# Kernel tuning notes

Measured on AMD Instinct MI355X. Metric: run time of the kernel, lower is better.

Reference implementation:

```python
import jax, jax.numpy as jnp
import numpy as np

B, L, E, H, D = 4, 2048, 2048, 16, 128
HALF = D // 2
EPS = 1e-6


def setup_inputs() -> dict:
    key = jax.random.key(0)
    ks = jax.random.split(key, 8)
    s = 1.0 / np.sqrt(E)
    x = jax.random.normal(ks[0], (B, L, E), dtype=jnp.float32)
    # causal boolean mask, True = attend
    attention_mask = jnp.tril(jnp.ones((L, L), dtype=bool))[None, None, :, :]
    attention_mask = jnp.broadcast_to(attention_mask, (B, 1, L, L))
    pos = jnp.arange(L, dtype=jnp.float32)[:, None]
    inv_freq = 1.0 / (10000.0 ** (jnp.arange(HALF, dtype=jnp.float32) / HALF))
    ang = pos * inv_freq[None, :]  # [L, HALF]
    cos = jnp.broadcast_to(jnp.cos(ang)[None], (B, L, HALF)).astype(jnp.float32)
    sin = jnp.broadcast_to(jnp.sin(ang)[None], (B, L, HALF)).astype(jnp.float32)
    Wq = jax.random.normal(ks[1], (H * D, E), dtype=jnp.float32) * s
    Wk = jax.random.normal(ks[2], (H * D, E), dtype=jnp.float32) * s
    Wv = jax.random.normal(ks[3], (H * D, E), dtype=jnp.float32) * s
    Wo = jax.random.normal(ks[4], (E, H * D), dtype=jnp.float32) * s
    q_norm_w = jnp.ones((D,), dtype=jnp.float32)
    k_norm_w = jnp.ones((D,), dtype=jnp.float32)
    return {"x": x, "attention_mask": attention_mask, "cos": cos, "sin": sin,
            "Wq": Wq, "Wk": Wk, "Wv": Wv, "Wo": Wo,
            "q_norm_w": q_norm_w, "k_norm_w": k_norm_w}


def _rmsnorm(t, w):
    # t: [B,H,L,D]; matches torch: x / sqrt(mean(x^2) + eps) * w
    ms = jnp.mean(t * t, axis=-1, keepdims=True)
    return w * (t * jax.lax.rsqrt(ms + EPS))


def _rope(t, cos, sin):
    # t: [B,H,L,D]; cos/sin: [B,L,HALF] -> [B,1,L,HALF]
    c = cos[:, None, :, :]
    s = sin[:, None, :, :]
    t1, t2 = t[..., :HALF], t[..., HALF:]
    return jnp.concatenate([t1 * c - t2 * s, t1 * s + t2 * c], axis=-1)


def reference(x, attention_mask, cos, sin, Wq, Wk, Wv, Wo, q_norm_w, k_norm_w):
    b, l, _ = x.shape
    q = (x @ Wq.T).reshape(b, l, H, D).transpose(0, 2, 1, 3)  # [B,H,L,D]
    k = (x @ Wk.T).reshape(b, l, H, D).transpose(0, 2, 1, 3)
    v = (x @ Wv.T).reshape(b, l, H, D).transpose(0, 2, 1, 3)
    q = _rope(_rmsnorm(q, q_norm_w), cos, sin)
    k = _rope(_rmsnorm(k, k_norm_w), cos, sin)
    scale = 1.0 / jnp.sqrt(jnp.asarray(D, dtype=x.dtype))
    scores = jnp.einsum('bhld,bhmd->bhlm', q, k) * scale  # [B,H,L,L]
    scores = jnp.where(attention_mask, scores, -jnp.inf)
    attn = jax.nn.softmax(scores, axis=-1)
    out = jnp.einsum('bhlm,bhmd->bhld', attn, v)  # [B,H,L,D]
    out = out.transpose(0, 2, 1, 3).reshape(b, l, H * D)
    return out @ Wo.T
```

## Files before the change

### kernel.cpp

```cpp
#include <hip/hip_runtime.h>
#include <hip/hip_bf16.h>
#include <stdint.h>

#define B_SZ 4
#define L_SEQ 2048
#define EMB 2048
#define NH 16
#define HD 128
#define BLROWS (B_SZ * L_SEQ)
#define BK 32

typedef __bf16 bf16;
typedef __bf16 bf16x8 __attribute__((ext_vector_type(8)));
typedef __bf16 bf16x4 __attribute__((ext_vector_type(4)));
typedef float f32x4 __attribute__((ext_vector_type(4)));

#define MFMA16(A, Bv, C) __builtin_amdgcn_mfma_f32_16x16x32_bf16(A, Bv, C, 0, 0, 0)

__device__ __forceinline__ void gll16(bf16* l, const bf16* g) {
  __builtin_amdgcn_global_load_lds(
      (const __attribute__((address_space(1))) unsigned int*)g,
      (__attribute__((address_space(3))) unsigned int*)l, 16, 0, 0);
}

__global__ __launch_bounds__(256) void f2bAll_kernel(
    const float* __restrict__ x, const float* __restrict__ w0,
    const float* __restrict__ w1, const float* __restrict__ w2,
    const float* __restrict__ w3, bf16* __restrict__ ox, bf16* __restrict__ o0,
    bf16* __restrict__ o1, bf16* __restrict__ o2, bf16* __restrict__ o3,
    int nx4, int nw4) {
  const int y = blockIdx.y;
  const float* in = (y == 0) ? x : (y == 1) ? w0 : (y == 2) ? w1
                    : (y == 3) ? w2 : w3;
  bf16* out = (y == 0) ? ox : (y == 1) ? o0 : (y == 2) ? o1
              : (y == 3) ? o2 : o3;
  const int n4 = (y == 0) ? nx4 : nw4;
  int i = blockIdx.x * blockDim.x + threadIdx.x;
  int stride = gridDim.x * blockDim.x;
  for (; i < n4; i += stride) {
    float4 v = ((const float4*)in)[i];
    bf16x4 o = {(bf16)v.x, (bf16)v.y, (bf16)v.z, (bf16)v.w};
    ((bf16x4*)out)[i] = o;
  }
}

template <int EPI, int BNT>
__global__ __launch_bounds__(512, 2) void gemm256(const bf16* __restrict__ A,
                                                  const bf16* __restrict__ Bm,
                                                  bf16* __restrict__ Cq,
                                                  bf16* __restrict__ Ck,
                                                  bf16* __restrict__ Cvt,
                                                  float* __restrict__ Cf,
                                                  int K) {
  constexpr int NB = BNT / 64;
  __shared__ bf16 Abuf[3][256 * BK];
  __shared__ bf16 Bbuf[3][BNT * BK];
  const int tid = threadIdx.x, lane = tid & 63, w = tid >> 6;
  const int wr = w >> 2, wc = w & 3;
  const int l15 = lane & 15;

  const int bx = blockIdx.x;
  const int bm = ((bx & 7) * 4 + ((bx >> 3) & 3)) * 256;
  const int bn = (bx >> 5) * BNT;
  const int NT = K / BK;

  const int idA0 = tid, idA1 = 512 + tid;
  const int ar0 = idA0 >> 2, ar1 = idA1 >> 2;
  const size_t aS0 = (size_t)(bm + ar0) * K + (((idA0 & 3) ^ ((ar0 >> 1) & 3)) * 8);
  const size_t aS1 = (size_t)(bm + ar1) * K + (((idA1 & 3) ^ ((ar1 >> 1) & 3)) * 8);
  const size_t bS0 = (size_t)(bn + ar0) * K + (((idA0 & 3) ^ ((ar0 >> 1) & 3)) * 8);
  const size_t bS1 = (size_t)(bn + ar1) * K + (((idA1 & 3) ^ ((ar1 >> 1) & 3)) * 8);
  const int ldsD0 = idA0 * 8, ldsD1 = idA1 * 8;

  const int eSw = ((lane >> 4) * 8) ^ (((l15 >> 1) & 3) << 3);
  int aoff[8], boff[NB];
#pragma unroll
  for (int m = 0; m < 8; m++) aoff[m] = (wr * 128 + m * 16 + l15) * BK + eSw;
#pragma unroll
  for (int n = 0; n < NB; n++) boff[n] = (wc * (BNT / 4) + n * 16 + l15) * BK + eSw;

  f32x4 acc[8][NB] = {};

  gll16(&Abuf[0][ldsD0], A + aS0);
  gll16(&Bbuf[0][ldsD0], Bm + bS0);
  gll16(&Abuf[0][ldsD1], A + aS1);
  if constexpr (BNT == 256) gll16(&Bbuf[0][ldsD1], Bm + bS1);
  gll16(&Abuf[1][ldsD0], A + aS0 + BK);
  gll16(&Bbuf[1][ldsD0], Bm + bS0 + BK);
  gll16(&Abuf[1][ldsD1], A + aS1 + BK);
  if constexpr (BNT == 256) gll16(&Bbuf[1][ldsD1], Bm + bS1 + BK);
  if constexpr (BNT == 256)
    asm volatile("s_waitcnt vmcnt(4)" ::: "memory");
  else
    asm volatile("s_waitcnt vmcnt(3)" ::: "memory");
  __builtin_amdgcn_s_barrier();
  asm volatile("" ::: "memory");

  int cur = 0, nxt = 2;
  for (int kt = 0; kt < NT; ++kt) {
    const bf16* __restrict__ Ab = Abuf[cur];
    const bf16* __restrict__ Bb = Bbuf[cur];
    const bool pre = (kt + 2 < NT);
    const size_t k2 = (size_t)(kt + 2) * BK;

    bf16x8 af[8], bq[NB];
#pragma unroll
    for (int m = 0; m < 8; m++) af[m] = *(const bf16x8*)&Ab[aoff[m]];
    bq[0] = *(const bf16x8*)&Bb[boff[0]];
    if constexpr (NB > 2) bq[1] = *(const bf16x8*)&Bb[boff[1]];
    if (pre) {
      gll16(&Abuf[nxt][ldsD0], A + aS0 + k2);
      gll16(&Bbuf[nxt][ldsD0], Bm + bS0 + k2);
    }
    asm volatile("s_waitcnt lgkmcnt(0)" ::: "memory");
    __builtin_amdgcn_sched_barrier(0);
    __builtin_amdgcn_s_setprio(1);
#pragma unroll
    for (int m = 0; m < 8; m++) acc[m][0] = MFMA16(af[m], bq[0], acc[m][0]);
    if constexpr (NB > 2) {
#pragma unroll
      for (int m = 0; m < 8; m++) acc[m][1] = MFMA16(af[m], bq[1], acc[m][1]);
    }
    __builtin_amdgcn_s_setprio(0);

    constexpr int n2 = (NB > 2) ? 2 : 1;
    bf16x8 b2 = *(const bf16x8*)&Bb[boff[n2]];
    bf16x8 b3;
    if constexpr (NB > 2) b3 = *(const bf16x8*)&Bb[boff[3]];
    if (pre) {
      gll16(&Abuf[nxt][ldsD1], A + aS1 + k2);
      if constexpr (BNT == 256) gll16(&Bbuf[nxt][ldsD1], Bm + bS1 + k2);
    }
    asm volatile("s_waitcnt lgkmcnt(0)" ::: "memory");
    __builtin_amdgcn_sched_barrier(0);
    __builtin_amdgcn_s_setprio(1);
#pragma unroll
    for (int m = 0; m < 8; m++) acc[m][n2] = MFMA16(af[m], b2, acc[m][n2]);
    if constexpr (NB > 2) {
#pragma unroll
      for (int m = 0; m < 8; m++) acc[m][3] = MFMA16(af[m], b3, acc[m][3]);
    }
    __builtin_amdgcn_s_setprio(0);

    if (kt < NT - 1) {
      if (pre) {
        if constexpr (BNT == 256)
          asm volatile("s_waitcnt vmcnt(4)" ::: "memory");
        else
          asm volatile("s_waitcnt vmcnt(3)" ::: "memory");
      } else {
        asm volatile("s_waitcnt vmcnt(0)" ::: "memory");
      }
      __builtin_amdgcn_s_barrier();
      asm volatile("" ::: "memory");
    }
    cur = (cur == 2) ? 0 : cur + 1;
    nxt = (nxt == 2) ? 0 : nxt + 1;
  }

  const int grow0 = bm + wr * 128 + (lane >> 4) * 4;
  const int gcol0 = bn + wc * (BNT / 4) + l15;
#pragma unroll
  for (int i = 0; i < 8; i++)
#pragma unroll
    for (int j = 0; j < NB; j++) {
      int grow = grow0 + i * 16;
      int gcol = gcol0 + j * 16;
      if (EPI == 1) {
#pragma unroll
        for (int r = 0; r < 4; r++)
          Cf[(size_t)(grow + r) * 2048 + gcol] = acc[i][j][r];
      } else {
        int mat = gcol >> 11, mcol = gcol & 2047;
        if (mat == 2) {
          int b = grow >> 11;
          bf16x4 pk = {(bf16)acc[i][j][0], (bf16)acc[i][j][1],
                       (bf16)acc[i][j][2], (bf16)acc[i][j][3]};
          *(bf16x4*)&Cvt[((size_t)(b * 2048 + mcol)) * 2048 + (grow & 2047)] = pk;
        } else {
          bf16* Cp = (mat == 0) ? Cq : Ck;
#pragma unroll
          for (int r = 0; r < 4; r++)
            Cp[(size_t)(grow + r) * 2048 + mcol] = (bf16)acc[i][j][r];
        }
      }
    }
}

__global__ __launch_bounds__(256) void normrope2_kernel(bf16* __restrict__ Tq,
                                                        bf16* __restrict__ Tk,
                                                        const float* __restrict__ wq,
                                                        const float* __restrict__ wk,
                                                        const float* __restrict__ cs,
                                                        const float* __restrict__ sn) {
  bf16* T = blockIdx.y ? Tk : Tq;
  const float* w = blockIdx.y ? wk : wq;
  int row = blockIdx.x * 4 + (threadIdx.x >> 6);
  int lane = threadIdx.x & 63;
  int bl = row >> 4;
  int h = row & 15;
  bf16* p = T + (size_t)bl * EMB + h * HD;
  float v1 = (float)p[lane];
  float v2 = (float)p[lane + 64];
  float ss = v1 * v1 + v2 * v2;
#pragma unroll
  for (int m = 32; m; m >>= 1) ss += __shfl_xor(ss, m, 64);
  float r = rsqrtf(ss * (1.0f / 128.0f) + 1e-6f);
  float n1 = v1 * r * w[lane];
  float n2 = v2 * r * w[lane + 64];
  float c = cs[(size_t)bl * 64 + lane];
  float s = sn[(size_t)bl * 64 + lane];
  p[lane]      = (bf16)(n1 * c - n2 * s);
  p[lane + 64] = (bf16)(n1 * s + n2 * c);
}

__device__ __forceinline__ void stage_kv(bf16* Ksb, bf16* Vsb,
                                         const bf16* gK, const bf16* gV,
                                         int kt, int w, int lane) {
#pragma unroll
  for (int i = 0; i < 4; i++) {
    int ck = i * 256 + w * 64 + lane;
    int kr = ck >> 4, kc = ck & 15;
    gll16(&Ksb[ck * 8], gK + (size_t)(kt * 64 + kr) * EMB + ((kc ^ (kr & 7)) * 8));
    int dr = ck >> 3, vc = ck & 7;
    gll16(&Vsb[ck * 8], gV + (size_t)dr * L_SEQ + kt * 64 + ((vc ^ (dr & 7)) * 8));
  }
}

__global__ __launch_bounds__(256) void fattn_kernel(const bf16* __restrict__ Q,
                                                    const bf16* __restrict__ K,
                                                    const bf16* __restrict__ Vt,
                                                    bf16* __restrict__ AO) {
  __shared__ bf16 Ks[2][64 * 128];
  __shared__ bf16 Vs[2][64 * 128];
  __shared__ bf16 Ps[4 * 16 * 64];
  const int tid = threadIdx.x, lane = tid & 63, w = tid >> 6;

  int id = blockIdx.x + blockIdx.y * 32;
  int bh = id & 63;
  int qt = 31 - (id >> 6);
  const int b = bh >> 4, h = bh & 15;
  const size_t base = (size_t)b * L_SEQ * EMB + h * HD;
  const bf16* gK = K + base;
  const bf16* gV = Vt + (size_t)(b * NH + h) * HD * L_SEQ;
  const int qrow0 = qt * 64 + w * 16;

  const float a_ = 0.08838834764831845f * 1.4426950408889634f;
  const float b_ = 12.0f * 1.4426950408889634f;

  bf16x8 qf[4];
  {
    const bf16* qp = Q + base + (size_t)(qrow0 + (lane & 15)) * EMB + ((lane >> 4) * 8);
#pragma unroll
    for (int c = 0; c < 4; c++) qf[c] = *(const bf16x8*)(qp + c * 32);
  }
  const bf16 one1 = (bf16)1.0f;
  const bf16x8 ones = {one1, one1, one1, one1, one1, one1, one1, one1};

  f32x4 O[8] = {};
  f32x4 lsum = {0.f, 0.f, 0.f, 0.f};
  const int qg0 = qrow0 + (lane >> 4) * 4;
  bf16* myP = Ps + w * 1024;

  stage_kv(Ks[0], Vs[0], gK, gV, 0, w, lane);
  asm volatile("s_waitcnt vmcnt(0)" ::: "memory");
  __builtin_amdgcn_s_barrier();
  asm volatile("" ::: "memory");

  for (int kt = 0; kt <= qt; kt++) {
    const int cur = kt & 1;
    if (kt < qt) stage_kv(Ks[cur ^ 1], Vs[cur ^ 1], gK, gV, kt + 1, w, lane);

    f32x4 S[4] = {};
    __builtin_amdgcn_s_setprio(1);
#pragma unroll
    for (int s = 0; s < 4; s++) {
      int row = s * 16 + (lane & 15);
#pragma unroll
      for (int c = 0; c < 4; c++) {
        int swc = (c * 4 + (lane >> 4)) ^ (row & 7);
        bf16x8 kf = *(const bf16x8*)&Ks[cur][row * 128 + swc * 8];
        S[s] = MFMA16(qf[c], kf, S[s]);
      }
    }
    __builtin_amdgcn_s_setprio(0);

    const bool diag = (kt == qt);
    const int prow = (lane >> 4) * 4;
#pragma unroll
    for (int s = 0; s < 4; s++) {
      int kg = kt * 64 + s * 16 + (lane & 15);
#pragma unroll
      for (int r = 0; r < 4; r++) {
        float e = exp2f(S[s][r] * a_ - b_);
        if (diag && kg > qg0 + r) e = 0.f;
        int row = prow + r;
        myP[(row * 64 + s * 16 + (lane & 15)) ^ ((row & 7) << 3)] = (bf16)e;
      }
    }
    bf16x8 pf[2];
#pragma unroll
    for (int kk = 0; kk < 2; kk++) {
      int row = lane & 15;
      int swc = (kk * 4 + (lane >> 4)) ^ (row & 7);
      pf[kk] = *(const bf16x8*)&myP[row * 64 + swc * 8];
    }
    __builtin_amdgcn_s_setprio(1);
    lsum = MFMA16(pf[0], ones, lsum);
    lsum = MFMA16(pf[1], ones, lsum);
#pragma unroll
    for (int ni = 0; ni < 8; ni++) {
#pragma unroll
      for (int kk = 0; kk < 2; kk++) {
        int drow = ni * 16 + (lane & 15);
        int swc = (kk * 4 + (lane >> 4)) ^ (drow & 7);
        bf16x8 vf = *(const bf16x8*)&Vs[cur][drow * 64 + swc * 8];
        O[ni] = MFMA16(pf[kk], vf, O[ni]);
      }
    }
    __builtin_amdgcn_s_setprio(0);

    asm volatile("s_waitcnt vmcnt(0)" ::: "memory");
    __builtin_amdgcn_s_barrier();
    asm volatile("" ::: "memory");
  }

#pragma unroll
  for (int ni = 0; ni < 8; ni++) {
#pragma unroll
    for (int r = 0; r < 4; r++) {
      float o = O[ni][r] / lsum[r];
      AO[(size_t)(b * L_SEQ + qg0 + r) * EMB + h * HD + ni * 16 + (lane & 15)] = (bf16)o;
    }
  }
}

extern "C" void kernel_launch(void* const* d_in, const int* in_sizes, int n_in,
                              void* d_out, int out_size, void* d_ws, size_t ws_size,
                              hipStream_t stream) {
  const float* x = (const float*)d_in[0];
  const float* cosp = (const float*)d_in[2];
  const float* sinp = (const float*)d_in[3];
  const float* Wq = (const float*)d_in[4];
  const float* Wk = (const float*)d_in[5];
  const float* Wv = (const float*)d_in[6];
  const float* Wo = (const float*)d_in[7];
  const float* qw = (const float*)d_in[8];
  const float* kw = (const float*)d_in[9];

  const size_t ACT = (size_t)BLROWS * EMB * sizeof(bf16);
  const size_t WGT = (size_t)EMB * EMB * sizeof(bf16);
  char* ws = (char*)d_ws;
  bf16* xb    = (bf16*)ws;          ws += ACT;
  bf16* WQKVb = (bf16*)ws;          ws += 3 * WGT;
  bf16* Wob   = (bf16*)ws;          ws += WGT;
  bf16* Qb    = (bf16*)ws;          ws += ACT;
  bf16* Kb    = (bf16*)ws;          ws += ACT;
  bf16* Vtb   = (bf16*)ws;          ws += ACT;
  bf16* AOb   = (bf16*)ws;          ws += ACT;

  f2bAll_kernel<<<dim3(512, 5), 256, 0, stream>>>(
      x, Wq, Wk, Wv, Wo, xb, WQKVb, WQKVb + (size_t)EMB * EMB,
      WQKVb + 2 * (size_t)EMB * EMB, Wob, BLROWS * EMB / 4, EMB * EMB / 4);

  gemm256<0, 256><<<768, 512, 0, stream>>>(xb, WQKVb, Qb, Kb, Vtb, nullptr, EMB);

  normrope2_kernel<<<dim3(BLROWS * NH / 4, 2), 256, 0, stream>>>(Qb, Kb, qw, kw,
                                                                 cosp, sinp);

  fattn_kernel<<<dim3(32, B_SZ * NH), 256, 0, stream>>>(Qb, Kb, Vtb, AOb);

  gemm256<1, 128><<<512, 512, 0, stream>>>(AOb, Wob, nullptr, nullptr, nullptr,
                                           (float*)d_out, EMB);
}
```

Baseline: 458.7 us.

## Use BK=64 double-buffered QKV GEMM with wider swizzle and fewer barriers

```diff
diff --git a/kernel.cpp b/kernel.cpp
--- a/kernel.cpp
+++ b/kernel.cpp
@@ -44,15 +44,133 @@
   }
 }
 
-template <int EPI, int BNT>
-__global__ __launch_bounds__(512, 2) void gemm256(const bf16* __restrict__ A,
+__global__ __launch_bounds__(512, 2) void gemmQKV64(const bf16* __restrict__ A,
+                                                    const bf16* __restrict__ Bm,
+                                                    bf16* __restrict__ Cq,
+                                                    bf16* __restrict__ Ck,
+                                                    bf16* __restrict__ Cvt,
+                                                    int K) {
+  __shared__ bf16 Abuf[2][256 * 64];
+  __shared__ bf16 Bbuf[2][256 * 64];
+  const int tid = threadIdx.x, lane = tid & 63, w = tid >> 6;
+  const int wr = w >> 2, wc = w & 3;
+  const int l15 = lane & 15, grp = lane >> 4;
+
+  const int bx = blockIdx.x;
+  const int bm = ((bx & 7) * 4 + ((bx >> 3) & 3)) * 256;
+  const int bn = (bx >> 5) * 256;
+  const int NT = K >> 6;
+
+  size_t sAg[4], sBg[4];
+  int sdst[4];
+#pragma unroll
+  for (int g = 0; g < 4; g++) {
+    int id = g * 512 + tid;
+    int row = id >> 3, c = id & 7;
+    int scol = (c ^ (row & 7)) * 8;
+    sAg[g] = (size_t)(bm + row) * K + scol;
+    sBg[g] = (size_t)(bn + row) * K + scol;
+    sdst[g] = id * 8;
+  }
+
+  int aoff[8][2], boff[4][2];
+#pragma unroll
+  for (int m = 0; m < 8; m++)
+#pragma unroll
+    for (int ks = 0; ks < 2; ks++) {
+      int row = wr * 128 + m * 16 + l15;
+      int cl = ks * 4 + grp;
+      aoff[m][ks] = row * 64 + ((cl ^ (row & 7)) * 8);
+    }
+#pragma unroll
+  for (int n = 0; n < 4; n++)
+#pragma unroll
+    for (int ks = 0; ks < 2; ks++) {
+      int row = wc * 64 + n * 16 + l15;
+      int cl = ks * 4 + grp;
+      boff[n][ks] = row * 64 + ((cl ^ (row & 7)) * 8);
+    }
+
+  f32x4 acc[8][4] = {};
+
+#pragma unroll
+  for (int g = 0; g < 4; g++) {
+    gll16(&Abuf[0][sdst[g]], A + sAg[g]);
+    gll16(&Bbuf[0][sdst[g]], Bm + sBg[g]);
+  }
+  asm volatile("s_waitcnt vmcnt(0)" ::: "memory");
+  __builtin_amdgcn_s_barrier();
+  asm volatile("" ::: "memory");
+
+  for (int t = 0; t < NT; ++t) {
+    const bf16* __restrict__ Ab = Abuf[t & 1];
+    const bf16* __restrict__ Bb = Bbuf[t & 1];
+    bf16* __restrict__ An = Abuf[(t + 1) & 1];
+    bf16* __restrict__ Bn = Bbuf[(t + 1) & 1];
+    const size_t k1 = (size_t)(t + 1) << 6;
+    const bool pre = (t + 1 < NT);
+
+    if (pre) {
+#pragma unroll
+      for (int g = 0; g < 4; g++) {
+        gll16(&An[sdst[g]], A + sAg[g] + k1);
+        gll16(&Bn[sdst[g]], Bm + sBg[g] + k1);
+      }
+    }
+
+#pragma unroll
+    for (int ks = 0; ks < 2; ks++) {
+      bf16x8 af[8], bq[4];
+#pragma unroll
+      for (int m = 0; m < 8; m++) af[m] = *(const bf16x8*)&Ab[aoff[m][ks]];
+#pragma unroll
+      for (int n = 0; n < 4; n++) bq[n] = *(const bf16x8*)&Bb[boff[n][ks]];
+      asm volatile("s_waitcnt lgkmcnt(0)" ::: "memory");
+      __builtin_amdgcn_sched_barrier(0);
+      __builtin_amdgcn_s_setprio(1);
+#pragma unroll
+      for (int n = 0; n < 4; n++)
+#pragma unroll
+        for (int m = 0; m < 8; m++)
+          acc[m][n] = MFMA16(af[m], bq[n], acc[m][n]);
+      __builtin_amdgcn_s_setprio(0);
+    }
+
+    if (t < NT - 1) {
+      asm volatile("s_waitcnt vmcnt(0)" ::: "memory");
+      __builtin_amdgcn_s_barrier();
+      asm volatile("" ::: "memory");
+    }
+  }
+
+  const int grow0 = bm + wr * 128 + grp * 4;
+  const int gcol0 = bn + wc * 64 + l15;
+#pragma unroll
+  for (int i = 0; i < 8; i++)
+#pragma unroll
+    for (int j = 0; j < 4; j++) {
+      int grow = grow0 + i * 16;
+      int gcol = gcol0 + j * 16;
+      int mat = gcol >> 11, mcol = gcol & 2047;
+      if (mat == 2) {
+        int b = grow >> 11;
+        bf16x4 pk = {(bf16)acc[i][j][0], (bf16)acc[i][j][1],
+                     (bf16)acc[i][j][2], (bf16)acc[i][j][3]};
+        *(bf16x4*)&Cvt[((size_t)(b * 2048 + mcol)) * 2048 + (grow & 2047)] = pk;
+      } else {
+        bf16* Cp = (mat == 0) ? Cq : Ck;
+#pragma unroll
+        for (int r = 0; r < 4; r++)
+          Cp[(size_t)(grow + r) * 2048 + mcol] = (bf16)acc[i][j][r];
+      }
+    }
+}
+
+__global__ __launch_bounds__(512, 2) void gemmOut(const bf16* __restrict__ A,
                                                   const bf16* __restrict__ Bm,
-                                                  bf16* __restrict__ Cq,
-                                                  bf16* __restrict__ Ck,
-                                                  bf16* __restrict__ Cvt,
                                                   float* __restrict__ Cf,
                                                   int K) {
-  constexpr int NB = BNT / 64;
+  constexpr int BNT = 128, NB = 2;
   __shared__ bf16 Abuf[3][256 * BK];
   __shared__ bf16 Bbuf[3][BNT * BK];
   const int tid = threadIdx.x, lane = tid & 63, w = tid >> 6;
@@ -69,7 +187,6 @@
   const size_t aS0 = (size_t)(bm + ar0) * K + (((idA0 & 3) ^ ((ar0 >> 1) & 3)) * 8);
   const size_t aS1 = (size_t)(bm + ar1) * K + (((idA1 & 3) ^ ((ar1 >> 1) & 3)) * 8);
   const size_t bS0 = (size_t)(bn + ar0) * K + (((idA0 & 3) ^ ((ar0 >> 1) & 3)) * 8);
-  const size_t bS1 = (size_t)(bn + ar1) * K + (((idA1 & 3) ^ ((ar1 >> 1) & 3)) * 8);
   const int ldsD0 = idA0 * 8, ldsD1 = idA1 * 8;
 
   const int eSw = ((lane >> 4) * 8) ^ (((l15 >> 1) & 3) << 3);
@@ -84,15 +201,10 @@
   gll16(&Abuf[0][ldsD0], A + aS0);
   gll16(&Bbuf[0][ldsD0], Bm + bS0);
   gll16(&Abuf[0][ldsD1], A + aS1);
-  if constexpr (BNT == 256) gll16(&Bbuf[0][ldsD1], Bm + bS1);
   gll16(&Abuf[1][ldsD0], A + aS0 + BK);
   gll16(&Bbuf[1][ldsD0], Bm + bS0 + BK);
   gll16(&Abuf[1][ldsD1], A + aS1 + BK);
-  if constexpr (BNT == 256) gll16(&Bbuf[1][ldsD1], Bm + bS1 + BK);
-  if constexpr (BNT == 256)
-    asm volatile("s_waitcnt vmcnt(4)" ::: "memory");
-  else
-    asm volatile("s_waitcnt vmcnt(3)" ::: "memory");
+  asm volatile("s_waitcnt vmcnt(3)" ::: "memory");
   __builtin_amdgcn_s_barrier();
   asm volatile("" ::: "memory");
 
@@ -107,7 +219,6 @@
 #pragma unroll
     for (int m = 0; m < 8; m++) af[m] = *(const bf16x8*)&Ab[aoff[m]];
     bq[0] = *(const bf16x8*)&Bb[boff[0]];
-    if constexpr (NB > 2) bq[1] = *(const bf16x8*)&Bb[boff[1]];
     if (pre) {
       gll16(&Abuf[nxt][ldsD0], A + aS0 + k2);
       gll16(&Bbuf[nxt][ldsD0], Bm + bS0 + k2);
@@ -117,40 +228,22 @@
     __builtin_amdgcn_s_setprio(1);
 #pragma unroll
     for (int m = 0; m < 8; m++) acc[m][0] = MFMA16(af[m], bq[0], acc[m][0]);
-    if constexpr (NB > 2) {
-#pragma unroll
-      for (int m = 0; m < 8; m++) acc[m][1] = MFMA16(af[m], bq[1], acc[m][1]);
-    }
     __builtin_amdgcn_s_setprio(0);
 
-    constexpr int n2 = (NB > 2) ? 2 : 1;
-    bf16x8 b2 = *(const bf16x8*)&Bb[boff[n2]];
-    bf16x8 b3;
-    if constexpr (NB > 2) b3 = *(const bf16x8*)&Bb[boff[3]];
-    if (pre) {
-      gll16(&Abuf[nxt][ldsD1], A + aS1 + k2);
-      if constexpr (BNT == 256) gll16(&Bbuf[nxt][ldsD1], Bm + bS1 + k2);
-    }
+    bf16x8 b2 = *(const bf16x8*)&Bb[boff[1]];
+    if (pre) gll16(&Abuf[nxt][ldsD1], A + aS1 + k2);
     asm volatile("s_waitcnt lgkmcnt(0)" ::: "memory");
     __builtin_amdgcn_sched_barrier(0);
     __builtin_amdgcn_s_setprio(1);
 #pragma unroll
-    for (int m = 0; m < 8; m++) acc[m][n2] = MFMA16(af[m], b2, acc[m][n2]);
-    if constexpr (NB > 2) {
-#pragma unroll
-      for (int m = 0; m < 8; m++) acc[m][3] = MFMA16(af[m], b3, acc[m][3]);
-    }
+    for (int m = 0; m < 8; m++) acc[m][1] = MFMA16(af[m], b2, acc[m][1]);
     __builtin_amdgcn_s_setprio(0);
 
     if (kt < NT - 1) {
-      if (pre) {
-        if constexpr (BNT == 256)
-          asm volatile("s_waitcnt vmcnt(4)" ::: "memory");
-        else
-          asm volatile("s_waitcnt vmcnt(3)" ::: "memory");
-      } else {
+      if (pre)
+        asm volatile("s_waitcnt vmcnt(3)" ::: "memory");
+      else
         asm volatile("s_waitcnt vmcnt(0)" ::: "memory");
-      }
       __builtin_amdgcn_s_barrier();
       asm volatile("" ::: "memory");
     }
@@ -166,24 +259,9 @@
     for (int j = 0; j < NB; j++) {
       int grow = grow0 + i * 16;
       int gcol = gcol0 + j * 16;
-      if (EPI == 1) {
-#pragma unroll
-        for (int r = 0; r < 4; r++)
-          Cf[(size_t)(grow + r) * 2048 + gcol] = acc[i][j][r];
-      } else {
-        int mat = gcol >> 11, mcol = gcol & 2047;
-        if (mat == 2) {
-          int b = grow >> 11;
-          bf16x4 pk = {(bf16)acc[i][j][0], (bf16)acc[i][j][1],
-                       (bf16)acc[i][j][2], (bf16)acc[i][j][3]};
-          *(bf16x4*)&Cvt[((size_t)(b * 2048 + mcol)) * 2048 + (grow & 2047)] = pk;
-        } else {
-          bf16* Cp = (mat == 0) ? Cq : Ck;
-#pragma unroll
-          for (int r = 0; r < 4; r++)
-            Cp[(size_t)(grow + r) * 2048 + mcol] = (bf16)acc[i][j][r];
-        }
-      }
+#pragma unroll
+      for (int r = 0; r < 4; r++)
+        Cf[(size_t)(grow + r) * 2048 + gcol] = acc[i][j][r];
     }
 }
 
@@ -363,13 +441,12 @@
       x, Wq, Wk, Wv, Wo, xb, WQKVb, WQKVb + (size_t)EMB * EMB,
       WQKVb + 2 * (size_t)EMB * EMB, Wob, BLROWS * EMB / 4, EMB * EMB / 4);
 
-  gemm256<0, 256><<<768, 512, 0, stream>>>(xb, WQKVb, Qb, Kb, Vtb, nullptr, EMB);
+  gemmQKV64<<<768, 512, 0, stream>>>(xb, WQKVb, Qb, Kb, Vtb, EMB);
 
   normrope2_kernel<<<dim3(BLROWS * NH / 4, 2), 256, 0, stream>>>(Qb, Kb, qw, kw,
                                                                  cosp, sinp);
 
   fattn_kernel<<<dim3(32, B_SZ * NH), 256, 0, stream>>>(Qb, Kb, Vtb, AOb);
 
-  gemm256<1, 128><<<512, 512, 0, stream>>>(AOb, Wob, nullptr, nullptr, nullptr,
-                                           (float*)d_out, EMB);
-}
+  gemmOut<<<512, 512, 0, stream>>>(AOb, Wob, (float*)d_out, EMB);
+}
```

After: 471.1 us. +2.7%, slower.
